# Performance work log

Hardware: AMD Instinct MI355X
Metric: run time of the kernel (lower is better)

## Reference

```python
import jax, jax.numpy as jnp
import numpy as np
from jax import lax

B_SZ = 64
D_MODEL = 768
D_INNER = 1536   # expand * d_model
D_STATE = 16
D_CONV = 4
DT_RANK = 48     # ceil(768/16)
ROWS, COLS = 16, 16
L = ROWS * COLS
LN_EPS = 1e-5


def setup_inputs() -> dict:
    key = jax.random.key(0)
    ks = jax.random.split(key, 16)
    def nrm(k, shape, s):
        return jax.random.normal(k, shape, jnp.float32) * s
    # A_log init as in Mamba: log(arange(1..d_state)) tiled over d_inner
    A_log = jnp.log(jnp.tile(jnp.arange(1, D_STATE + 1, dtype=jnp.float32)[None, :], (D_INNER, 1)))
    # dt bias init: inverse-softplus of dt ~ LogUniform(1e-3, 1e-1)
    def dt_bias_init(k):
        u = jax.random.uniform(k, (D_INNER,), jnp.float32)
        dt = jnp.exp(u * (np.log(0.1) - np.log(0.001)) + np.log(0.001))
        return dt + jnp.log(-jnp.expm1(-dt))
    dt_std = DT_RANK ** -0.5
    return {
        "hidden_states": jax.random.normal(ks[0], (B_SZ, L, D_MODEL), jnp.float32),
        "in_proj_w": nrm(ks[1], (2 * D_INNER, D_MODEL), 0.02),
        "conv_w": nrm(ks[2], (D_INNER, D_CONV), 0.2),
        "conv_bias": nrm(ks[3], (D_INNER,), 0.1),
        "conv_w_b": nrm(ks[4], (D_INNER, D_CONV), 0.2),
        "conv_bias_b": nrm(ks[5], (D_INNER,), 0.1),
        "x_proj_w": nrm(ks[6], (DT_RANK + 2 * D_STATE, D_INNER), 0.02),
        "x_proj_w_b": nrm(ks[7], (DT_RANK + 2 * D_STATE, D_INNER), 0.02),
        "dt_proj_w": jax.random.uniform(ks[8], (D_INNER, DT_RANK), jnp.float32, -dt_std, dt_std),
        "dt_proj_w_b": jax.random.uniform(ks[9], (D_INNER, DT_RANK), jnp.float32, -dt_std, dt_std),
        "dt_bias": dt_bias_init(ks[10]),
        "dt_bias_b": dt_bias_init(ks[11]),
        "A_log": A_log,
        "A_b_log": A_log,
        "Dp": jnp.ones((D_INNER,), jnp.float32),
        "Dp_b": jnp.ones((D_INNER,), jnp.float32),
        "ln_gamma": jnp.ones((D_INNER,), jnp.float32),
        "ln_beta": jnp.zeros((D_INNER,), jnp.float32),
        "out_proj_w": nrm(ks[12], (D_MODEL, D_INNER), 0.02),
    }


def _causal_conv_silu(x, w, b):
    # x: (B, D, L); depthwise causal conv (left-pad K-1) + SiLU
    y = lax.conv_general_dilated(x, w[:, None, :], (1,), [(D_CONV - 1, 0)],
                                 dimension_numbers=("NCH", "OIH", "NCH"),
                                 feature_group_count=D_INNER)
    return jax.nn.silu(y + b[None, :, None])


def _selective_scan(u, dt, A_log, Bm, Cm, dt_bias):
    # u, dt: (B, D, Lr); Bm, Cm: (B, N, Lr)
    A = -jnp.exp(A_log)                                     # (D, N)
    delta = jax.nn.softplus(dt + dt_bias[None, :, None])    # (B, D, Lr)
    dA = jnp.exp(jnp.einsum("bdl,dn->lbdn", delta, A))     # (Lr, B, D, N)
    dBu = jnp.einsum("bdl,bnl,bdl->lbdn", delta, Bm, u)    # (Lr, B, D, N)
    C_l = jnp.moveaxis(Cm, -1, 0)                           # (Lr, B, N)
    def step(h, inp):
        dA_t, dBu_t, C_t = inp
        h = dA_t * h + dBu_t
        return h, jnp.einsum("bdn,bn->bd", h, C_t)
    h0 = jnp.zeros(dA.shape[1:], dA.dtype)
    _, ys = lax.scan(step, h0, (dA, dBu, C_l))
    return jnp.moveaxis(ys, 0, -1)                          # (B, D, Lr)


def _direction(x, conv_w, conv_bias, x_proj_w, dt_proj_w, dt_bias, A_log, Dp):
    xc = _causal_conv_silu(x, conv_w, conv_bias)            # (B, D, L)
    x_comp = xc.reshape(-1, D_INNER, ROWS, COLS).mean(axis=3)  # (B, D, ROWS)
    x_dbl = jnp.einsum("bdl,ed->ble", x_comp, x_proj_w)    # (B, ROWS, R+2N)
    dt, Bm, Cm = jnp.split(x_dbl, [DT_RANK, DT_RANK + D_STATE], axis=-1)
    dt = jnp.einsum("blr,dr->bdl", dt, dt_proj_w)          # (B, D, ROWS)
    Bm = jnp.moveaxis(Bm, 1, 2)                             # (B, N, ROWS)
    Cm = jnp.moveaxis(Cm, 1, 2)
    y = _selective_scan(x_comp, dt, A_log, Bm, Cm, dt_bias)
    return jnp.repeat(y, COLS, axis=2) + Dp[None, :, None] * xc  # (B, D, L)


def reference(hidden_states, in_proj_w, conv_w, conv_bias, conv_w_b, conv_bias_b,
              x_proj_w, x_proj_w_b, dt_proj_w, dt_proj_w_b, dt_bias, dt_bias_b,
              A_log, A_b_log, Dp, Dp_b, ln_gamma, ln_beta, out_proj_w):
    xz = jnp.einsum("bld,ed->bel", hidden_states, in_proj_w)  # (B, 2*Di, L)
    x, z = jnp.split(xz, 2, axis=1)
    out_f = _direction(x, conv_w, conv_bias, x_proj_w, dt_proj_w, dt_bias, A_log, Dp)
    out_b = _direction(x[:, :, ::-1], conv_w_b, conv_bias_b, x_proj_w_b, dt_proj_w_b, dt_bias_b, A_b_log, Dp_b)
    comb = jnp.moveaxis((out_f + out_b[:, :, ::-1]) * 0.5, 1, 2)  # (B, L, Di)
    mu = comb.mean(-1, keepdims=True)
    var = comb.var(-1, keepdims=True)
    normed = (comb - mu) * lax.rsqrt(var + LN_EPS) * ln_gamma + ln_beta
    gated = normed * jax.nn.silu(jnp.moveaxis(z, 1, 2))
    return jnp.einsum("bld,od->blo", gated, out_proj_w)       # (B, L, d_model)
```

## Files before the change

### kernel.cpp

```cpp
#include <hip/hip_runtime.h>
#include <cstdint>
#include <cstddef>

typedef __bf16 bf16_t;
typedef __attribute__((ext_vector_type(2))) __bf16 bf16x2;
typedef __attribute__((ext_vector_type(8))) __bf16 bf16x8;
typedef __attribute__((ext_vector_type(4))) float f32x4;

#define NB     64
#define LSEQ   256
#define DM     768
#define DI     1536
#define NSTATE 16
#define NROWS  16
#define RANK   48

#define BF16_PROBE 0x3F803F80u

__device__ __forceinline__ float bf2f(bf16_t v) { return (float)v; }

__device__ __forceinline__ float ldp(const void* p, size_t i, bool isbf) {
  return isbf ? (float)((const bf16_t*)p)[i] : ((const float*)p)[i];
}

__device__ __forceinline__ float silu_f(float x) {
  const float e = __expf(-fabsf(x));
  return (x >= 0.f) ? (x / (1.f + e)) : (x * e / (1.f + e));
}

__device__ __forceinline__ void async16(const bf16_t* g, bf16_t* l) {
  __builtin_amdgcn_global_load_lds(
      (const __attribute__((address_space(1))) void*)g,
      (__attribute__((address_space(3))) void*)l, 16, 0, 0);
}

__global__ __launch_bounds__(256) void cvt_kernel(
    const void* __restrict__ in, bf16_t* __restrict__ out, int n8,
    const uint32_t* __restrict__ probe)
{
  const int i = blockIdx.x * 256 + threadIdx.x;
  if (i >= n8) return;
  if (probe[0] == BF16_PROBE) {
    ((bf16x8*)out)[i] = ((const bf16x8*)in)[i];
  } else {
    const float* f = (const float*)in + (size_t)i * 8;
    f32x4 lo = *(const f32x4*)f, hi = *(const f32x4*)(f + 4);
    ((bf16x8*)out)[i] = (bf16x8){(bf16_t)lo.x, (bf16_t)lo.y, (bf16_t)lo.z, (bf16_t)lo.w,
                                 (bf16_t)hi.x, (bf16_t)hi.y, (bf16_t)hi.z, (bf16_t)hi.w};
  }
}

#define LDS_IDX(ab, db, half) (((ab) << 2) + ((db) << 1) + (half))

#define STAGE(ab, db, half, kt) do {                                          \
    const int _kt = ((kt) < NT) ? (kt) : (NT - 1);                            \
    const bf16_t* _g = (ab) ? B : A;                                          \
    const size_t _rb = ((ab) ? bn : bm) + (size_t)((half) * 128);             \
    bf16_t* _l = &sm[LDS_IDX(ab, db, half)][0];                               \
    _Pragma("unroll")                                                         \
    for (int _j = 0; _j < 2; _j++) {                                          \
      const int _c = wave * 2 + _j;                                           \
      async16(_g + (_rb + _c * 8 + srow) * (size_t)K + (size_t)_kt * 64 + scol,\
              _l + _c * 512);                                                 \
    }                                                                         \
  } while (0)

#define LOAD_A(db, mg) do {                                                   \
    _Pragma("unroll")                                                         \
    for (int _t = 0; _t < 2; _t++) {                                          \
      const int _mt = (mg) * 2 + _t;                                          \
      const int _lr = _mt * 32 + wm * 16 + r;                                 \
      const bf16_t* _b = &sm[LDS_IDX(0, db, _mt >> 2)][(_lr & 127) * 64];     \
      _Pragma("unroll")                                                       \
      for (int _s = 0; _s < 2; _s++)                                          \
        af[_t][_s] = *(const bf16x8*)&_b[(((_s * 4 + quad) ^ r7) * 8)];       \
    }                                                                         \
  } while (0)

#define LOAD_B(db) do {                                                       \
    _Pragma("unroll")                                                         \
    for (int _nt = 0; _nt < 4; _nt++) {                                       \
      const int _lr = _nt * 64 + wn * 16 + r;                                 \
      const bf16_t* _b = &sm[LDS_IDX(1, db, _lr >> 7)][(_lr & 127) * 64];     \
      _Pragma("unroll")                                                       \
      for (int _s = 0; _s < 2; _s++)                                          \
        bfr[_nt][_s] = *(const bf16x8*)&_b[(((_s * 4 + quad) ^ r7) * 8)];     \
    }                                                                         \
  } while (0)

#define MFMA16(mg) do {                                                       \
    __builtin_amdgcn_s_setprio(1);                                            \
    _Pragma("unroll")                                                         \
    for (int _t = 0; _t < 2; _t++)                                            \
    _Pragma("unroll")                                                         \
    for (int _nt = 0; _nt < 4; _nt++)                                         \
    _Pragma("unroll")                                                         \
    for (int _s = 0; _s < 2; _s++)                                            \
      acc[(mg) * 2 + _t][_nt] = __builtin_amdgcn_mfma_f32_16x16x32_bf16(      \
          af[_t][_s], bfr[_nt][_s], acc[(mg) * 2 + _t][_nt], 0, 0, 0);        \
    __builtin_amdgcn_s_setprio(0);                                            \
  } while (0)

#define BAR()    __builtin_amdgcn_s_barrier()
#define WAITL0() asm volatile("s_waitcnt lgkmcnt(0)" ::: "memory")
#define WAITV6() asm volatile("s_waitcnt vmcnt(6)" ::: "memory")

__global__ __launch_bounds__(512, 2) void gemm256_kernel(
    const bf16_t* __restrict__ A, const bf16_t* __restrict__ B,
    void* __restrict__ C, int M, int N, int K, int cIsF32)
{
  __shared__ bf16_t sm[8][8192];
  const int tid  = threadIdx.x;
  const int wave = tid >> 6, lane = tid & 63;
  const int wm = wave >> 2, wn = wave & 3;
  const int r = lane & 15, quad = lane >> 4, r7 = lane & 7;
  const int srow = lane >> 3;
  const int scol = ((lane & 7) ^ srow) * 8;
  const int NT = K >> 6;

  const int nwg  = gridDim.x * gridDim.y;
  const int orig = blockIdx.y * gridDim.x + blockIdx.x;
  const int swz  = (orig & 7) * (nwg >> 3) + (orig >> 3);
  const size_t bm = (size_t)(swz / gridDim.x) * 256;
  const size_t bn = (size_t)(swz % gridDim.x) * 256;

  f32x4 acc[8][4];
#pragma unroll
  for (int i = 0; i < 8; i++)
#pragma unroll
    for (int j = 0; j < 4; j++) acc[i][j] = (f32x4){0.f, 0.f, 0.f, 0.f};

  bf16x8 af[2][2];
  bf16x8 bfr[4][2];

  STAGE(1, 0, 0, 0);  STAGE(1, 0, 1, 0);  STAGE(0, 0, 0, 0);  STAGE(0, 0, 1, 0);
  asm volatile("s_waitcnt vmcnt(4)" ::: "memory");
  STAGE(1, 1, 0, 1);  STAGE(1, 1, 1, 1);  STAGE(0, 1, 0, 1);
  WAITV6();
  BAR();

  const int NP = NT >> 1;
  for (int i = 0; i < NP; ++i) {
    const int t1 = 2 * i + 1, t2 = 2 * i + 2, t3 = 2 * i + 3;
    LOAD_B(0); LOAD_A(0, 0); STAGE(0, 1, 1, t1);
    BAR(); WAITL0(); MFMA16(0); BAR();

    LOAD_A(0, 1); STAGE(1, 0, 0, t2);
    BAR(); WAITL0(); MFMA16(1); BAR();

    LOAD_A(0, 2); STAGE(1, 0, 1, t2);
    BAR(); WAITL0(); MFMA16(2); BAR();

    LOAD_A(0, 3); STAGE(0, 0, 0, t2);
    WAITV6();
    BAR(); WAITL0(); MFMA16(3); BAR();

    LOAD_B(1); LOAD_A(1, 0); STAGE(0, 0, 1, t2);
    BAR(); WAITL0(); MFMA16(0); BAR();

    LOAD_A(1, 1); STAGE(1, 1, 0, t3);
    BAR(); WAITL0(); MFMA16(1); BAR();

    LOAD_A(1, 2); STAGE(1, 1, 1, t3);
    BAR(); WAITL0(); MFMA16(2); BAR();

    LOAD_A(1, 3); STAGE(0, 1, 0, t3);
    WAITV6();
    BAR(); WAITL0(); MFMA16(3); BAR();
  }

  const int col = lane & 15;
  const int rb4 = quad * 4;
#pragma unroll
  for (int mt = 0; mt < 8; mt++)
#pragma unroll
    for (int nt = 0; nt < 4; nt++)
#pragma unroll
      for (int v = 0; v < 4; v++) {
        const size_t m = bm + mt * 32 + wm * 16 + rb4 + v;
        const size_t n = bn + nt * 64 + wn * 16 + col;
        const size_t ci = m * (size_t)N + n;
        if (cIsF32) ((float*)C)[ci] = acc[mt][nt][v];
        else        ((bf16_t*)C)[ci] = (bf16_t)acc[mt][nt][v];
      }
}

__global__ __launch_bounds__(256) void conv_kernel(
    const bf16_t* __restrict__ xz,
    const void* __restrict__ cw_f, const void* __restrict__ cb_f,
    const void* __restrict__ cw_b, const void* __restrict__ cb_b,
    bf16_t* __restrict__ xc_f, bf16_t* __restrict__ xc_b,
    float* __restrict__ comp_f, float* __restrict__ comp_b,
    const uint32_t* __restrict__ probe)
{
  const bool isbf = (probe[0] == BF16_PROBE);
  const int dir = blockIdx.y;
  int bi = blockIdx.x;
  const int chunk = bi & 3;
  bi >>= 2;
  const int b = bi / 3;
  const int pblk = bi % 3;
  const int d0 = (pblk * 256 + threadIdx.x) * 2;
  const void* cw = dir ? cw_b : cw_f;
  const void* cb = dir ? cb_b : cb_f;
  bf16_t* xc = dir ? xc_b : xc_f;
  float* comp = dir ? comp_b : comp_f;

  const float w00 = ldp(cw, d0 * 4 + 0, isbf), w01 = ldp(cw, d0 * 4 + 1, isbf),
              w02 = ldp(cw, d0 * 4 + 2, isbf), w03 = ldp(cw, d0 * 4 + 3, isbf);
  const float w10 = ldp(cw, (d0 + 1) * 4 + 0, isbf), w11 = ldp(cw, (d0 + 1) * 4 + 1, isbf),
              w12 = ldp(cw, (d0 + 1) * 4 + 2, isbf), w13 = ldp(cw, (d0 + 1) * 4 + 3, isbf);
  const float bias0 = ldp(cb, d0, isbf), bias1 = ldp(cb, d0 + 1, isbf);

  float a3 = 0.f, a2 = 0.f, a1 = 0.f;
  float c3 = 0.f, c2 = 0.f, c1 = 0.f;
  const int lr0 = chunk * 64;
  if (lr0 >= 3) {
#pragma unroll
    for (int i = 3; i >= 1; --i) {
      const int lrp = lr0 - i;
      const int l = dir ? (LSEQ - 1 - lrp) : lrp;
      bf16x2 xv = *(const bf16x2*)(xz + ((size_t)b * LSEQ + l) * (2 * DI) + d0);
      a3 = a2; a2 = a1; a1 = (float)xv.x;
      c3 = c2; c2 = c1; c1 = (float)xv.y;
    }
  }

  float s0 = 0.f, s1 = 0.f;
  for (int lr = lr0; lr < lr0 + 64; ++lr) {
    const int l = dir ? (LSEQ - 1 - lr) : lr;
    bf16x2 xv = *(const bf16x2*)(xz + ((size_t)b * LSEQ + l) * (2 * DI) + d0);
    const float x0 = (float)xv.x, x1 = (float)xv.y;
    float y0 = silu_f(bias0 + w00 * a3 + w01 * a2 + w02 * a1 + w03 * x0);
    float y1 = silu_f(bias1 + w10 * c3 + w11 * c2 + w12 * c1 + w13 * x1);
    a3 = a2; a2 = a1; a1 = x0;
    c3 = c2; c2 = c1; c1 = x1;
    *(bf16x2*)(xc + ((size_t)b * LSEQ + lr) * DI + d0) = (bf16x2){(bf16_t)y0, (bf16_t)y1};
    s0 += y0; s1 += y1;
    if ((lr & 15) == 15) {
      size_t ci = ((size_t)b * NROWS + (lr >> 4)) * DI + d0;
      comp[ci]     = s0 * (1.f / 16.f);
      comp[ci + 1] = s1 * (1.f / 16.f);
      s0 = 0.f; s1 = 0.f;
    }
  }
}

__global__ __launch_bounds__(256) void xproj_kernel(
    const float* __restrict__ comp_f, const float* __restrict__ comp_b,
    const void* __restrict__ w_f, const void* __restrict__ w_b,
    float* __restrict__ xd_f, float* __restrict__ xd_b,
    const uint32_t* __restrict__ probe)
{
  const bool isbf = (probe[0] == BF16_PROBE);
  const int dir = blockIdx.y;
  const int row = blockIdx.x;
  const float* comp = dir ? comp_b : comp_f;
  const void* W = dir ? w_b : w_f;
  float* out = dir ? xd_b : xd_f;

  __shared__ float xrow[DI];
  for (int i = threadIdx.x; i < DI; i += 256) xrow[i] = comp[(size_t)row * DI + i];
  __syncthreads();

  const int wave = threadIdx.x >> 6, lane = threadIdx.x & 63;
  for (int oo = 0; oo < 20; ++oo) {
    const int o = wave * 20 + oo;
    float s = 0.f;
#pragma unroll
    for (int j = 0; j < 24; ++j) {
      const int k = lane + 64 * j;
      s += xrow[k] * ldp(W, (size_t)o * DI + k, isbf);
    }
    for (int off = 32; off; off >>= 1) s += __shfl_down(s, off);
    if (lane == 0) out[(size_t)row * 80 + o] = s;
  }
}

__global__ __launch_bounds__(256) void scan_kernel(
    const float* __restrict__ xd_fg, const float* __restrict__ xd_bg,
    const float* comp_f, const float* comp_b,
    const void* __restrict__ dtw_f, const void* __restrict__ dtw_b,
    const void* __restrict__ dtb_f, const void* __restrict__ dtb_b,
    const void* __restrict__ Al_f, const void* __restrict__ Al_b,
    float* y_fg, float* y_bg,
    const uint32_t* __restrict__ probe)
{
  const bool isbf = (probe[0] == BF16_PROBE);
  const int dir = blockIdx.y;
  const int b = blockIdx.x / 6;
  const int d = (blockIdx.x % 6) * 256 + threadIdx.x;
  const float* xd_g = dir ? xd_bg : xd_fg;
  const float* comp = dir ? comp_b : comp_f;
  const void* dtw = dir ? dtw_b : dtw_f;
  const void* dtb = dir ? dtb_b : dtb_f;
  const void* Al  = dir ? Al_b : Al_f;
  float* y = dir ? y_bg : y_fg;

  __shared__ float xd[NROWS * 80];
  for (int i = threadIdx.x; i < NROWS * 80; i += 256) xd[i] = xd_g[(size_t)b * (NROWS * 80) + i];
  __syncthreads();

  float dt[NROWS];
#pragma unroll
  for (int l = 0; l < NROWS; l++) dt[l] = 0.f;
  for (int r = 0; r < RANK; r++) {
    const float w = ldp(dtw, (size_t)d * RANK + r, isbf);
#pragma unroll
    for (int l = 0; l < NROWS; l++) dt[l] += xd[l * 80 + r] * w;
  }

  float A[NSTATE];
#pragma unroll
  for (int n = 0; n < NSTATE; n++) A[n] = -__expf(ldp(Al, (size_t)d * NSTATE + n, isbf));
  const float bias = ldp(dtb, d, isbf);

  float h[NSTATE];
#pragma unroll
  for (int n = 0; n < NSTATE; n++) h[n] = 0.f;

  for (int l = 0; l < NROWS; l++) {
    const float u = comp[((size_t)b * NROWS + l) * DI + d];
    const float dv = dt[l] + bias;
    const float delta = (dv > 15.f) ? dv : log1pf(__expf(dv));
    const float du = delta * u;
    float yv = 0.f;
#pragma unroll
    for (int n = 0; n < NSTATE; n++) {
      const float hn = __expf(delta * A[n]) * h[n] + du * xd[l * 80 + RANK + n];
      h[n] = hn;
      yv += hn * xd[l * 80 + RANK + NSTATE + n];
    }
    y[((size_t)b * NROWS + l) * DI + d] = yv;
  }
}

__global__ __launch_bounds__(256) void combine_kernel(
    const float* __restrict__ y_f, const float* __restrict__ y_b,
    bf16_t* xcg_f,
    const bf16_t* __restrict__ xc_b,
    const bf16_t* __restrict__ xz,
    const void* __restrict__ Dp, const void* __restrict__ Dp_b,
    const void* __restrict__ gamma, const void* __restrict__ beta,
    const uint32_t* __restrict__ probe)
{
  const bool isbf = (probe[0] == BF16_PROBE);
  const int m = blockIdx.x;
  const int b = m >> 8, l = m & 255;
  const int lr = LSEQ - 1 - l;
  const int tid = threadIdx.x;

  float v[6];
  float sum = 0.f, sq = 0.f;
#pragma unroll
  for (int i = 0; i < 6; i++) {
    const int d = tid + i * 256;
    const float cf = bf2f(xcg_f[((size_t)b * LSEQ + l) * DI + d]);
    const float cb = bf2f(xc_b[((size_t)b * LSEQ + lr) * DI + d]);
    const float vf = y_f[((size_t)b * NROWS + (l >> 4)) * DI + d] + ldp(Dp, d, isbf) * cf;
    const float vb = y_b[((size_t)b * NROWS + (lr >> 4)) * DI + d] + ldp(Dp_b, d, isbf) * cb;
    const float c = 0.5f * (vf + vb);
    v[i] = c; sum += c; sq += c * c;
  }
  for (int off = 32; off; off >>= 1) {
    sum += __shfl_down(sum, off);
    sq  += __shfl_down(sq, off);
  }
  __shared__ float rs[4], rq[4];
  if ((tid & 63) == 0) { rs[tid >> 6] = sum; rq[tid >> 6] = sq; }
  __syncthreads();
  const float S  = rs[0] + rs[1] + rs[2] + rs[3];
  const float SQ = rq[0] + rq[1] + rq[2] + rq[3];
  const float mu = S * (1.f / (float)DI);
  const float var = fmaxf(SQ * (1.f / (float)DI) - mu * mu, 0.f);
  const float rstd = rsqrtf(var + 1e-5f);
#pragma unroll
  for (int i = 0; i < 6; i++) {
    const int d = tid + i * 256;
    const float nrm = (v[i] - mu) * rstd * ldp(gamma, d, isbf) + ldp(beta, d, isbf);
    const float z = bf2f(xz[((size_t)b * LSEQ + l) * (2 * DI) + DI + d]);
    xcg_f[(size_t)m * DI + d] = (bf16_t)(nrm * silu_f(z));
  }
}

extern "C" void kernel_launch(void* const* d_in, const int* in_sizes, int n_in,
                              void* d_out, int out_size, void* d_ws, size_t ws_size,
                              hipStream_t stream)
{
  (void)in_sizes; (void)n_in; (void)out_size; (void)ws_size;
  const void* H     = d_in[0];
  const void* Win   = d_in[1];
  const void* cw_f  = d_in[2];
  const void* cb_f  = d_in[3];
  const void* cw_b  = d_in[4];
  const void* cb_b  = d_in[5];
  const void* xpw_f = d_in[6];
  const void* xpw_b = d_in[7];
  const void* dtw_f = d_in[8];
  const void* dtw_b = d_in[9];
  const void* dtb_f = d_in[10];
  const void* dtb_b = d_in[11];
  const void* Al_f  = d_in[12];
  const void* Al_b  = d_in[13];
  const void* Dp    = d_in[14];
  const void* Dp_b  = d_in[15];
  const void* gam   = d_in[16];
  const void* bet   = d_in[17];
  const void* Wout  = d_in[18];
  const uint32_t* probe = (const uint32_t*)d_in[14];

  const size_t M = (size_t)NB * LSEQ;
  char* ws = (char*)d_ws;
  bf16_t* xz    = (bf16_t*)ws;  ws += M * (2 * DI) * sizeof(bf16_t);
  bf16_t* xc_f  = (bf16_t*)ws;  ws += M * DI * sizeof(bf16_t);
  bf16_t* xc_b  = (bf16_t*)ws;  ws += M * DI * sizeof(bf16_t);
  float* comp_f = (float*)ws;   ws += (size_t)NB * NROWS * DI * sizeof(float);
  float* comp_b = (float*)ws;   ws += (size_t)NB * NROWS * DI * sizeof(float);
  float* xd_f   = (float*)ws;   ws += (size_t)NB * NROWS * 80 * sizeof(float);
  float* xd_b   = (float*)ws;   ws += (size_t)NB * NROWS * 80 * sizeof(float);
  bf16_t* Hb    = (bf16_t*)ws;  ws += M * DM * sizeof(bf16_t);
  bf16_t* Winb  = (bf16_t*)ws;  ws += (size_t)(2 * DI) * DM * sizeof(bf16_t);
  bf16_t* Woutb = (bf16_t*)ws;  ws += (size_t)DM * DI * sizeof(bf16_t);

  cvt_kernel<<<(int)((M * DM / 8 + 255) / 256), 256, 0, stream>>>(H, Hb, (int)(M * DM / 8), probe);
  cvt_kernel<<<(2 * DI * DM / 8 + 255) / 256, 256, 0, stream>>>(Win, Winb, 2 * DI * DM / 8, probe);
  cvt_kernel<<<(DM * DI / 8 + 255) / 256, 256, 0, stream>>>(Wout, Woutb, DM * DI / 8, probe);

  gemm256_kernel<<<dim3(2 * DI / 256, M / 256), 512, 0, stream>>>(
      Hb, Winb, xz, (int)M, 2 * DI, DM, 0);

  conv_kernel<<<dim3(768, 2), 256, 0, stream>>>(
      xz, cw_f, cb_f, cw_b, cb_b, xc_f, xc_b, comp_f, comp_b, probe);

  xproj_kernel<<<dim3(NB * NROWS, 2), 256, 0, stream>>>(
      comp_f, comp_b, xpw_f, xpw_b, xd_f, xd_b, probe);

  scan_kernel<<<dim3(NB * (DI / 256), 2), 256, 0, stream>>>(
      xd_f, xd_b, comp_f, comp_b, dtw_f, dtw_b, dtb_f, dtb_b, Al_f, Al_b,
      comp_f, comp_b, probe);

  combine_kernel<<<dim3(NB * LSEQ), 256, 0, stream>>>(
      comp_f, comp_b, xc_f, xc_b, xz, Dp, Dp_b, gam, bet, probe);

  gemm256_kernel<<<dim3(DM / 256, M / 256), 512, 0, stream>>>(
      xc_f, Woutb, d_out, (int)M, DM, DI, 1);
}
```

Before: 478.1 us.

## Fuse causal conv and row pooling into in-projection GEMM epilogue

The in-projection GEMM epilogue now transposes the x-half tile through LDS and runs the forward and backward depthwise causal conv, SiLU and 16-step pooling directly, writing xc and comp. The z-half is stored as a compact bf16 buffer, so the full xz intermediate and the separate conv kernel are gone. The dt_proj weights are also pre-transposed to fp32 so the scan reads them coalesced. In exchange the GEMM epilogue gets heavier and serial per thread, and the enlarged LDS footprint (about 132KB) may reduce occupancy relative to the two-blocks-per-CU launch bound.

```diff
diff --git a/kernel.cpp b/kernel.cpp
--- a/kernel.cpp
+++ b/kernel.cpp
@@ -6,6 +6,7 @@
 typedef __attribute__((ext_vector_type(2))) __bf16 bf16x2;
 typedef __attribute__((ext_vector_type(8))) __bf16 bf16x8;
 typedef __attribute__((ext_vector_type(4))) float f32x4;
+typedef __attribute__((ext_vector_type(2))) float f32x2;
 
 #define NB     64
 #define LSEQ   256
@@ -48,6 +49,17 @@
     ((bf16x8*)out)[i] = (bf16x8){(bf16_t)lo.x, (bf16_t)lo.y, (bf16_t)lo.z, (bf16_t)lo.w,
                                  (bf16_t)hi.x, (bf16_t)hi.y, (bf16_t)hi.z, (bf16_t)hi.w};
   }
+}
+
+__global__ __launch_bounds__(256) void dtwt_kernel(
+    const void* __restrict__ dtw, float* __restrict__ out,
+    const uint32_t* __restrict__ probe)
+{
+  const bool isbf = (probe[0] == BF16_PROBE);
+  const int i = blockIdx.x * 256 + threadIdx.x;
+  if (i >= RANK * DI) return;
+  const int r = i / DI, d = i - r * DI;
+  out[i] = ldp(dtw, (size_t)d * RANK + r, isbf);
 }
 
 #define LDS_IDX(ab, db, half) (((ab) << 2) + ((db) << 1) + (half))
@@ -107,9 +119,17 @@
 
 __global__ __launch_bounds__(512, 2) void gemm256_kernel(
     const bf16_t* __restrict__ A, const bf16_t* __restrict__ B,
-    void* __restrict__ C, int M, int N, int K, int cIsF32)
-{
-  __shared__ bf16_t sm[8][8192];
+    void* __restrict__ C, int M, int N, int K, int mode,
+    bf16_t* __restrict__ xc_f, bf16_t* __restrict__ xc_b,
+    float* __restrict__ comp_f, float* __restrict__ comp_b,
+    const void* __restrict__ cw_f, const void* __restrict__ cb_f,
+    const void* __restrict__ cw_b, const void* __restrict__ cb_b,
+    const uint32_t* __restrict__ probe)
+{
+  __shared__ __align__(16) char smraw[256 * 258 * 2];
+  typedef bf16_t row8k_t[8192];
+  row8k_t* sm = (row8k_t*)smraw;
+
   const int tid  = threadIdx.x;
   const int wave = tid >> 6, lane = tid & 63;
   const int wm = wave >> 2, wn = wave & 3;
@@ -169,79 +189,109 @@
     BAR(); WAITL0(); MFMA16(3); BAR();
   }
 
-  const int col = lane & 15;
+  const int col16 = lane & 15;
   const int rb4 = quad * 4;
-#pragma unroll
-  for (int mt = 0; mt < 8; mt++)
-#pragma unroll
-    for (int nt = 0; nt < 4; nt++)
-#pragma unroll
-      for (int v = 0; v < 4; v++) {
-        const size_t m = bm + mt * 32 + wm * 16 + rb4 + v;
-        const size_t n = bn + nt * 64 + wn * 16 + col;
-        const size_t ci = m * (size_t)N + n;
-        if (cIsF32) ((float*)C)[ci] = acc[mt][nt][v];
-        else        ((bf16_t*)C)[ci] = (bf16_t)acc[mt][nt][v];
+
+  if (mode == 0) {
+#pragma unroll
+    for (int mt = 0; mt < 8; mt++)
+#pragma unroll
+      for (int nt = 0; nt < 4; nt++)
+#pragma unroll
+        for (int v = 0; v < 4; v++) {
+          const size_t m = bm + mt * 32 + wm * 16 + rb4 + v;
+          const size_t n = bn + nt * 64 + wn * 16 + col16;
+          ((float*)C)[m * (size_t)N + n] = acc[mt][nt][v];
+        }
+  } else if (bn >= (size_t)DI) {
+    bf16_t* zb = (bf16_t*)C;
+    const size_t zc = bn - DI;
+#pragma unroll
+    for (int mt = 0; mt < 8; mt++)
+#pragma unroll
+      for (int nt = 0; nt < 4; nt++)
+#pragma unroll
+        for (int v = 0; v < 4; v++) {
+          const size_t m = bm + mt * 32 + wm * 16 + rb4 + v;
+          zb[m * DI + zc + nt * 64 + wn * 16 + col16] = (bf16_t)acc[mt][nt][v];
+        }
+  } else {
+    asm volatile("s_waitcnt vmcnt(0)" ::: "memory");
+    __syncthreads();
+    bf16_t* xt = (bf16_t*)smraw;
+#pragma unroll
+    for (int mt = 0; mt < 8; mt++) {
+      const int mrow = mt * 32 + wm * 16 + rb4;
+#pragma unroll
+      for (int nt = 0; nt < 4; nt++) {
+        const int ccol = nt * 64 + wn * 16 + col16;
+        bf16_t* qp = &xt[ccol * 258 + mrow];
+        *(bf16x2*)qp       = (bf16x2){(bf16_t)acc[mt][nt][0], (bf16_t)acc[mt][nt][1]};
+        *(bf16x2*)(qp + 2) = (bf16x2){(bf16_t)acc[mt][nt][2], (bf16_t)acc[mt][nt][3]};
       }
-}
-
-__global__ __launch_bounds__(256) void conv_kernel(
-    const bf16_t* __restrict__ xz,
-    const void* __restrict__ cw_f, const void* __restrict__ cb_f,
-    const void* __restrict__ cw_b, const void* __restrict__ cb_b,
-    bf16_t* __restrict__ xc_f, bf16_t* __restrict__ xc_b,
-    float* __restrict__ comp_f, float* __restrict__ comp_b,
-    const uint32_t* __restrict__ probe)
-{
-  const bool isbf = (probe[0] == BF16_PROBE);
-  const int dir = blockIdx.y;
-  int bi = blockIdx.x;
-  const int chunk = bi & 3;
-  bi >>= 2;
-  const int b = bi / 3;
-  const int pblk = bi % 3;
-  const int d0 = (pblk * 256 + threadIdx.x) * 2;
-  const void* cw = dir ? cw_b : cw_f;
-  const void* cb = dir ? cb_b : cb_f;
-  bf16_t* xc = dir ? xc_b : xc_f;
-  float* comp = dir ? comp_b : comp_f;
-
-  const float w00 = ldp(cw, d0 * 4 + 0, isbf), w01 = ldp(cw, d0 * 4 + 1, isbf),
-              w02 = ldp(cw, d0 * 4 + 2, isbf), w03 = ldp(cw, d0 * 4 + 3, isbf);
-  const float w10 = ldp(cw, (d0 + 1) * 4 + 0, isbf), w11 = ldp(cw, (d0 + 1) * 4 + 1, isbf),
-              w12 = ldp(cw, (d0 + 1) * 4 + 2, isbf), w13 = ldp(cw, (d0 + 1) * 4 + 3, isbf);
-  const float bias0 = ldp(cb, d0, isbf), bias1 = ldp(cb, d0 + 1, isbf);
-
-  float a3 = 0.f, a2 = 0.f, a1 = 0.f;
-  float c3 = 0.f, c2 = 0.f, c1 = 0.f;
-  const int lr0 = chunk * 64;
-  if (lr0 >= 3) {
-#pragma unroll
-    for (int i = 3; i >= 1; --i) {
-      const int lrp = lr0 - i;
-      const int l = dir ? (LSEQ - 1 - lrp) : lrp;
-      bf16x2 xv = *(const bf16x2*)(xz + ((size_t)b * LSEQ + l) * (2 * DI) + d0);
-      a3 = a2; a2 = a1; a1 = (float)xv.x;
-      c3 = c2; c2 = c1; c1 = (float)xv.y;
     }
-  }
-
-  float s0 = 0.f, s1 = 0.f;
-  for (int lr = lr0; lr < lr0 + 64; ++lr) {
-    const int l = dir ? (LSEQ - 1 - lr) : lr;
-    bf16x2 xv = *(const bf16x2*)(xz + ((size_t)b * LSEQ + l) * (2 * DI) + d0);
-    const float x0 = (float)xv.x, x1 = (float)xv.y;
-    float y0 = silu_f(bias0 + w00 * a3 + w01 * a2 + w02 * a1 + w03 * x0);
-    float y1 = silu_f(bias1 + w10 * c3 + w11 * c2 + w12 * c1 + w13 * x1);
-    a3 = a2; a2 = a1; a1 = x0;
-    c3 = c2; c2 = c1; c1 = x1;
-    *(bf16x2*)(xc + ((size_t)b * LSEQ + lr) * DI + d0) = (bf16x2){(bf16_t)y0, (bf16_t)y1};
-    s0 += y0; s1 += y1;
-    if ((lr & 15) == 15) {
-      size_t ci = ((size_t)b * NROWS + (lr >> 4)) * DI + d0;
-      comp[ci]     = s0 * (1.f / 16.f);
-      comp[ci + 1] = s1 * (1.f / 16.f);
-      s0 = 0.f; s1 = 0.f;
+    __syncthreads();
+
+    const bool isbf = (probe[0] == BF16_PROBE);
+    const int p  = tid & 127;
+    const int qq = tid >> 7;
+    const int c0 = p * 2;
+    const int r0 = qq * 64;
+    const int dg = (int)bn + c0;
+    const int bidx = (int)(bm >> 8);
+    const bf16_t* x0 = &xt[c0 * 258];
+    const bf16_t* x1 = &xt[(c0 + 1) * 258];
+
+#pragma unroll
+    for (int dir = 0; dir < 2; ++dir) {
+      const void* cw = dir ? cw_b : cw_f;
+      const void* cb = dir ? cb_b : cb_f;
+      bf16_t* xc  = dir ? xc_b : xc_f;
+      float* comp = dir ? comp_b : comp_f;
+      const float wa0 = ldp(cw, (size_t)dg * 4 + 0, isbf),
+                  wa1 = ldp(cw, (size_t)dg * 4 + 1, isbf),
+                  wa2 = ldp(cw, (size_t)dg * 4 + 2, isbf),
+                  wa3 = ldp(cw, (size_t)dg * 4 + 3, isbf);
+      const float wb0 = ldp(cw, (size_t)(dg + 1) * 4 + 0, isbf),
+                  wb1 = ldp(cw, (size_t)(dg + 1) * 4 + 1, isbf),
+                  wb2 = ldp(cw, (size_t)(dg + 1) * 4 + 2, isbf),
+                  wb3 = ldp(cw, (size_t)(dg + 1) * 4 + 3, isbf);
+      const float ba = ldp(cb, dg, isbf), bb = ldp(cb, dg + 1, isbf);
+      float a1 = 0.f, a2 = 0.f, a3 = 0.f, b1 = 0.f, b2 = 0.f, b3 = 0.f;
+      if (r0 > 0) {
+        if (dir == 0) {
+          a1 = (float)x0[r0 - 1]; a2 = (float)x0[r0 - 2]; a3 = (float)x0[r0 - 3];
+          b1 = (float)x1[r0 - 1]; b2 = (float)x1[r0 - 2]; b3 = (float)x1[r0 - 3];
+        } else {
+          a1 = (float)x0[256 - r0]; a2 = (float)x0[257 - r0]; a3 = (float)x0[258 - r0];
+          b1 = (float)x1[256 - r0]; b2 = (float)x1[257 - r0]; b3 = (float)x1[258 - r0];
+        }
+      }
+      float sa = 0.f, sb = 0.f;
+      for (int rr = 0; rr < 64; rr += 2) {
+        const int lr = r0 + rr;
+        const int row = dir ? (254 - lr) : lr;
+        const bf16x2 va = *(const bf16x2*)&x0[row];
+        const bf16x2 vb = *(const bf16x2*)&x1[row];
+        const float xaf = dir ? (float)va.y : (float)va.x;
+        const float xas = dir ? (float)va.x : (float)va.y;
+        const float xbf = dir ? (float)vb.y : (float)vb.x;
+        const float xbs = dir ? (float)vb.x : (float)vb.y;
+        const float ya0 = silu_f(ba + wa0 * a3 + wa1 * a2 + wa2 * a1 + wa3 * xaf);
+        const float yb0 = silu_f(bb + wb0 * b3 + wb1 * b2 + wb2 * b1 + wb3 * xbf);
+        a3 = a2; a2 = a1; a1 = xaf;  b3 = b2; b2 = b1; b1 = xbf;
+        const float ya1 = silu_f(ba + wa0 * a3 + wa1 * a2 + wa2 * a1 + wa3 * xas);
+        const float yb1 = silu_f(bb + wb0 * b3 + wb1 * b2 + wb2 * b1 + wb3 * xbs);
+        a3 = a2; a2 = a1; a1 = xas;  b3 = b2; b2 = b1; b1 = xbs;
+        *(bf16x2*)&xc[((size_t)(bm + lr)) * DI + dg]     = (bf16x2){(bf16_t)ya0, (bf16_t)yb0};
+        *(bf16x2*)&xc[((size_t)(bm + lr + 1)) * DI + dg] = (bf16x2){(bf16_t)ya1, (bf16_t)yb1};
+        sa += ya0 + ya1; sb += yb0 + yb1;
+        if ((rr & 15) == 14) {
+          *(f32x2*)&comp[((size_t)bidx * NROWS + (lr >> 4)) * DI + dg] =
+              (f32x2){sa * (1.f / 16.f), sb * (1.f / 16.f)};
+          sa = 0.f; sb = 0.f;
+        }
+      }
     }
   }
 }
@@ -280,7 +330,7 @@
 __global__ __launch_bounds__(256) void scan_kernel(
     const float* __restrict__ xd_fg, const float* __restrict__ xd_bg,
     const float* comp_f, const float* comp_b,
-    const void* __restrict__ dtw_f, const void* __restrict__ dtw_b,
+    const float* __restrict__ dtwT_f, const float* __restrict__ dtwT_b,
     const void* __restrict__ dtb_f, const void* __restrict__ dtb_b,
     const void* __restrict__ Al_f, const void* __restrict__ Al_b,
     float* y_fg, float* y_bg,
@@ -292,7 +342,7 @@
   const int d = (blockIdx.x % 6) * 256 + threadIdx.x;
   const float* xd_g = dir ? xd_bg : xd_fg;
   const float* comp = dir ? comp_b : comp_f;
-  const void* dtw = dir ? dtw_b : dtw_f;
+  const float* dtwT = dir ? dtwT_b : dtwT_f;
   const void* dtb = dir ? dtb_b : dtb_f;
   const void* Al  = dir ? Al_b : Al_f;
   float* y = dir ? y_bg : y_fg;
@@ -305,7 +355,7 @@
 #pragma unroll
   for (int l = 0; l < NROWS; l++) dt[l] = 0.f;
   for (int r = 0; r < RANK; r++) {
-    const float w = ldp(dtw, (size_t)d * RANK + r, isbf);
+    const float w = dtwT[(size_t)r * DI + d];
 #pragma unroll
     for (int l = 0; l < NROWS; l++) dt[l] += xd[l * 80 + r] * w;
   }
@@ -339,7 +389,7 @@
     const float* __restrict__ y_f, const float* __restrict__ y_b,
     bf16_t* xcg_f,
     const bf16_t* __restrict__ xc_b,
-    const bf16_t* __restrict__ xz,
+    const bf16_t* __restrict__ zb,
     const void* __restrict__ Dp, const void* __restrict__ Dp_b,
     const void* __restrict__ gamma, const void* __restrict__ beta,
     const uint32_t* __restrict__ probe)
@@ -378,7 +428,7 @@
   for (int i = 0; i < 6; i++) {
     const int d = tid + i * 256;
     const float nrm = (v[i] - mu) * rstd * ldp(gamma, d, isbf) + ldp(beta, d, isbf);
-    const float z = bf2f(xz[((size_t)b * LSEQ + l) * (2 * DI) + DI + d]);
+    const float z = bf2f(zb[(size_t)m * DI + d]);
     xcg_f[(size_t)m * DI + d] = (bf16_t)(nrm * silu_f(z));
   }
 }
@@ -411,7 +461,7 @@
 
   const size_t M = (size_t)NB * LSEQ;
   char* ws = (char*)d_ws;
-  bf16_t* xz    = (bf16_t*)ws;  ws += M * (2 * DI) * sizeof(bf16_t);
+  bf16_t* zb    = (bf16_t*)ws;  ws += M * DI * sizeof(bf16_t);
   bf16_t* xc_f  = (bf16_t*)ws;  ws += M * DI * sizeof(bf16_t);
   bf16_t* xc_b  = (bf16_t*)ws;  ws += M * DI * sizeof(bf16_t);
   float* comp_f = (float*)ws;   ws += (size_t)NB * NROWS * DI * sizeof(float);
@@ -421,27 +471,30 @@
   bf16_t* Hb    = (bf16_t*)ws;  ws += M * DM * sizeof(bf16_t);
   bf16_t* Winb  = (bf16_t*)ws;  ws += (size_t)(2 * DI) * DM * sizeof(bf16_t);
   bf16_t* Woutb = (bf16_t*)ws;  ws += (size_t)DM * DI * sizeof(bf16_t);
+  float* dtwT_f = (float*)ws;   ws += (size_t)RANK * DI * sizeof(float);
+  float* dtwT_b = (float*)ws;   ws += (size_t)RANK * DI * sizeof(float);
 
   cvt_kernel<<<(int)((M * DM / 8 + 255) / 256), 256, 0, stream>>>(H, Hb, (int)(M * DM / 8), probe);
   cvt_kernel<<<(2 * DI * DM / 8 + 255) / 256, 256, 0, stream>>>(Win, Winb, 2 * DI * DM / 8, probe);
   cvt_kernel<<<(DM * DI / 8 + 255) / 256, 256, 0, stream>>>(Wout, Woutb, DM * DI / 8, probe);
+  dtwt_kernel<<<(RANK * DI + 255) / 256, 256, 0, stream>>>(dtw_f, dtwT_f, probe);
+  dtwt_kernel<<<(RANK * DI + 255) / 256, 256, 0, stream>>>(dtw_b, dtwT_b, probe);
 
   gemm256_kernel<<<dim3(2 * DI / 256, M / 256), 512, 0, stream>>>(
-      Hb, Winb, xz, (int)M, 2 * DI, DM, 0);
-
-  conv_kernel<<<dim3(768, 2), 256, 0, stream>>>(
-      xz, cw_f, cb_f, cw_b, cb_b, xc_f, xc_b, comp_f, comp_b, probe);
+      Hb, Winb, zb, (int)M, 2 * DI, DM, 1,
+      xc_f, xc_b, comp_f, comp_b, cw_f, cb_f, cw_b, cb_b, probe);
 
   xproj_kernel<<<dim3(NB * NROWS, 2), 256, 0, stream>>>(
       comp_f, comp_b, xpw_f, xpw_b, xd_f, xd_b, probe);
 
   scan_kernel<<<dim3(NB * (DI / 256), 2), 256, 0, stream>>>(
-      xd_f, xd_b, comp_f, comp_b, dtw_f, dtw_b, dtb_f, dtb_b, Al_f, Al_b,
+      xd_f, xd_b, comp_f, comp_b, dtwT_f, dtwT_b, dtb_f, dtb_b, Al_f, Al_b,
       comp_f, comp_b, probe);
 
   combine_kernel<<<dim3(NB * LSEQ), 256, 0, stream>>>(
-      comp_f, comp_b, xc_f, xc_b, xz, Dp, Dp_b, gam, bet, probe);
+      comp_f, comp_b, xc_f, xc_b, zb, Dp, Dp_b, gam, bet, probe);
 
   gemm256_kernel<<<dim3(DM / 256, M / 256), 512, 0, stream>>>(
-      xc_f, Woutb, d_out, (int)M, DM, DI, 1);
-}
+      xc_f, Woutb, d_out, (int)M, DM, DI, 0,
+      nullptr, nullptr, nullptr, nullptr, nullptr, nullptr, nullptr, nullptr, probe);
+}
```

New measurement: 470.0 us. About the same (-1.7%).

## Split in-proj output into x/z buffers and fuse both conv directions into one pass

Applied to the files above, without the earlier changes.

The in-projection GEMM epilogue now writes the x half and z half into separate contiguous [M, DI] bf16 buffers. The conv kernel loads each x value once and computes both the forward and the reversed-direction causal conv from the same sliding window, halving its grid and its reads of x. The combine kernel reads z from the dense buffer. This cuts redundant global reads and improves stride, at the cost of a more complex conv loop with three extra halo iterations per chunk.

```diff
diff --git a/kernel.cpp b/kernel.cpp
--- a/kernel.cpp
+++ b/kernel.cpp
@@ -6,6 +6,7 @@
 typedef __attribute__((ext_vector_type(2))) __bf16 bf16x2;
 typedef __attribute__((ext_vector_type(8))) __bf16 bf16x8;
 typedef __attribute__((ext_vector_type(4))) float f32x4;
+typedef __attribute__((ext_vector_type(2))) float f32x2;
 
 #define NB     64
 #define LSEQ   256
@@ -107,7 +108,8 @@
 
 __global__ __launch_bounds__(512, 2) void gemm256_kernel(
     const bf16_t* __restrict__ A, const bf16_t* __restrict__ B,
-    void* __restrict__ C, int M, int N, int K, int cIsF32)
+    void* __restrict__ C, int M, int N, int K, int mode,
+    bf16_t* __restrict__ xb)
 {
   __shared__ bf16_t sm[8][8192];
   const int tid  = threadIdx.x;
@@ -169,24 +171,37 @@
     BAR(); WAITL0(); MFMA16(3); BAR();
   }
 
-  const int col = lane & 15;
+  const int col16 = lane & 15;
   const int rb4 = quad * 4;
-#pragma unroll
-  for (int mt = 0; mt < 8; mt++)
-#pragma unroll
-    for (int nt = 0; nt < 4; nt++)
-#pragma unroll
-      for (int v = 0; v < 4; v++) {
-        const size_t m = bm + mt * 32 + wm * 16 + rb4 + v;
-        const size_t n = bn + nt * 64 + wn * 16 + col;
-        const size_t ci = m * (size_t)N + n;
-        if (cIsF32) ((float*)C)[ci] = acc[mt][nt][v];
-        else        ((bf16_t*)C)[ci] = (bf16_t)acc[mt][nt][v];
-      }
+
+  if (mode == 0) {
+#pragma unroll
+    for (int mt = 0; mt < 8; mt++)
+#pragma unroll
+      for (int nt = 0; nt < 4; nt++)
+#pragma unroll
+        for (int v = 0; v < 4; v++) {
+          const size_t m = bm + mt * 32 + wm * 16 + rb4 + v;
+          const size_t n = bn + nt * 64 + wn * 16 + col16;
+          ((float*)C)[m * (size_t)N + n] = acc[mt][nt][v];
+        }
+  } else {
+    bf16_t* dst = (bn < (size_t)DI) ? xb : (bf16_t*)C;
+    const size_t cb0 = (bn < (size_t)DI) ? bn : bn - DI;
+#pragma unroll
+    for (int mt = 0; mt < 8; mt++)
+#pragma unroll
+      for (int nt = 0; nt < 4; nt++)
+#pragma unroll
+        for (int v = 0; v < 4; v++) {
+          const size_t m = bm + mt * 32 + wm * 16 + rb4 + v;
+          dst[m * DI + cb0 + nt * 64 + wn * 16 + col16] = (bf16_t)acc[mt][nt][v];
+        }
+  }
 }
 
 __global__ __launch_bounds__(256) void conv_kernel(
-    const bf16_t* __restrict__ xz,
+    const bf16_t* __restrict__ xb,
     const void* __restrict__ cw_f, const void* __restrict__ cb_f,
     const void* __restrict__ cw_b, const void* __restrict__ cb_b,
     bf16_t* __restrict__ xc_f, bf16_t* __restrict__ xc_b,
@@ -194,54 +209,77 @@
     const uint32_t* __restrict__ probe)
 {
   const bool isbf = (probe[0] == BF16_PROBE);
-  const int dir = blockIdx.y;
   int bi = blockIdx.x;
   const int chunk = bi & 3;
   bi >>= 2;
   const int b = bi / 3;
   const int pblk = bi % 3;
   const int d0 = (pblk * 256 + threadIdx.x) * 2;
-  const void* cw = dir ? cw_b : cw_f;
-  const void* cb = dir ? cb_b : cb_f;
-  bf16_t* xc = dir ? xc_b : xc_f;
-  float* comp = dir ? comp_b : comp_f;
-
-  const float w00 = ldp(cw, d0 * 4 + 0, isbf), w01 = ldp(cw, d0 * 4 + 1, isbf),
-              w02 = ldp(cw, d0 * 4 + 2, isbf), w03 = ldp(cw, d0 * 4 + 3, isbf);
-  const float w10 = ldp(cw, (d0 + 1) * 4 + 0, isbf), w11 = ldp(cw, (d0 + 1) * 4 + 1, isbf),
-              w12 = ldp(cw, (d0 + 1) * 4 + 2, isbf), w13 = ldp(cw, (d0 + 1) * 4 + 3, isbf);
-  const float bias0 = ldp(cb, d0, isbf), bias1 = ldp(cb, d0 + 1, isbf);
-
-  float a3 = 0.f, a2 = 0.f, a1 = 0.f;
-  float c3 = 0.f, c2 = 0.f, c1 = 0.f;
   const int lr0 = chunk * 64;
-  if (lr0 >= 3) {
-#pragma unroll
-    for (int i = 3; i >= 1; --i) {
-      const int lrp = lr0 - i;
-      const int l = dir ? (LSEQ - 1 - lrp) : lrp;
-      bf16x2 xv = *(const bf16x2*)(xz + ((size_t)b * LSEQ + l) * (2 * DI) + d0);
-      a3 = a2; a2 = a1; a1 = (float)xv.x;
-      c3 = c2; c2 = c1; c1 = (float)xv.y;
+
+  const float wf0a = ldp(cw_f, (size_t)d0 * 4 + 0, isbf),
+              wf1a = ldp(cw_f, (size_t)d0 * 4 + 1, isbf),
+              wf2a = ldp(cw_f, (size_t)d0 * 4 + 2, isbf),
+              wf3a = ldp(cw_f, (size_t)d0 * 4 + 3, isbf);
+  const float wf0c = ldp(cw_f, (size_t)(d0 + 1) * 4 + 0, isbf),
+              wf1c = ldp(cw_f, (size_t)(d0 + 1) * 4 + 1, isbf),
+              wf2c = ldp(cw_f, (size_t)(d0 + 1) * 4 + 2, isbf),
+              wf3c = ldp(cw_f, (size_t)(d0 + 1) * 4 + 3, isbf);
+  const float wb0a = ldp(cw_b, (size_t)d0 * 4 + 0, isbf),
+              wb1a = ldp(cw_b, (size_t)d0 * 4 + 1, isbf),
+              wb2a = ldp(cw_b, (size_t)d0 * 4 + 2, isbf),
+              wb3a = ldp(cw_b, (size_t)d0 * 4 + 3, isbf);
+  const float wb0c = ldp(cw_b, (size_t)(d0 + 1) * 4 + 0, isbf),
+              wb1c = ldp(cw_b, (size_t)(d0 + 1) * 4 + 1, isbf),
+              wb2c = ldp(cw_b, (size_t)(d0 + 1) * 4 + 2, isbf),
+              wb3c = ldp(cw_b, (size_t)(d0 + 1) * 4 + 3, isbf);
+  const float bfa = ldp(cb_f, d0, isbf), bfc = ldp(cb_f, d0 + 1, isbf);
+  const float bba = ldp(cb_b, d0, isbf), bbc = ldp(cb_b, d0 + 1, isbf);
+
+  const bf16_t* xrow = xb + (size_t)b * LSEQ * DI + d0;
+
+  float t0a = 0.f, t1a = 0.f, t2a = 0.f, t3a = 0.f;
+  float t0c = 0.f, t1c = 0.f, t2c = 0.f, t3c = 0.f;
+  if (lr0 > 0) {
+    bf16x2 v;
+    v = *(const bf16x2*)&xrow[(size_t)(lr0 - 3) * DI]; t1a = (float)v.x; t1c = (float)v.y;
+    v = *(const bf16x2*)&xrow[(size_t)(lr0 - 2) * DI]; t2a = (float)v.x; t2c = (float)v.y;
+    v = *(const bf16x2*)&xrow[(size_t)(lr0 - 1) * DI]; t3a = (float)v.x; t3c = (float)v.y;
+  }
+
+  float sfa = 0.f, sfc = 0.f;
+  float sba = 0.f, sbc = 0.f;
+  for (int l = lr0; l < lr0 + 67; ++l) {
+    float xa = 0.f, xcv = 0.f;
+    if (l < LSEQ) {
+      bf16x2 v = *(const bf16x2*)&xrow[(size_t)l * DI];
+      xa = (float)v.x; xcv = (float)v.y;
     }
-  }
-
-  float s0 = 0.f, s1 = 0.f;
-  for (int lr = lr0; lr < lr0 + 64; ++lr) {
-    const int l = dir ? (LSEQ - 1 - lr) : lr;
-    bf16x2 xv = *(const bf16x2*)(xz + ((size_t)b * LSEQ + l) * (2 * DI) + d0);
-    const float x0 = (float)xv.x, x1 = (float)xv.y;
-    float y0 = silu_f(bias0 + w00 * a3 + w01 * a2 + w02 * a1 + w03 * x0);
-    float y1 = silu_f(bias1 + w10 * c3 + w11 * c2 + w12 * c1 + w13 * x1);
-    a3 = a2; a2 = a1; a1 = x0;
-    c3 = c2; c2 = c1; c1 = x1;
-    *(bf16x2*)(xc + ((size_t)b * LSEQ + lr) * DI + d0) = (bf16x2){(bf16_t)y0, (bf16_t)y1};
-    s0 += y0; s1 += y1;
-    if ((lr & 15) == 15) {
-      size_t ci = ((size_t)b * NROWS + (lr >> 4)) * DI + d0;
-      comp[ci]     = s0 * (1.f / 16.f);
-      comp[ci + 1] = s1 * (1.f / 16.f);
-      s0 = 0.f; s1 = 0.f;
+    t0a = t1a; t1a = t2a; t2a = t3a; t3a = xa;
+    t0c = t1c; t1c = t2c; t2c = t3c; t3c = xcv;
+
+    if (l < lr0 + 64) {
+      const float ya = silu_f(bfa + wf0a * t0a + wf1a * t1a + wf2a * t2a + wf3a * t3a);
+      const float yc = silu_f(bfc + wf0c * t0c + wf1c * t1c + wf2c * t2c + wf3c * t3c);
+      *(bf16x2*)&xc_f[((size_t)b * LSEQ + l) * DI + d0] = (bf16x2){(bf16_t)ya, (bf16_t)yc};
+      sfa += ya; sfc += yc;
+      if ((l & 15) == 15) {
+        *(f32x2*)&comp_f[((size_t)b * NROWS + (l >> 4)) * DI + d0] =
+            (f32x2){sfa * (1.f / 16.f), sfc * (1.f / 16.f)};
+        sfa = 0.f; sfc = 0.f;
+      }
+    }
+    if (l >= lr0 + 3) {
+      const int j = 258 - l;
+      const float ya = silu_f(bba + wb0a * t3a + wb1a * t2a + wb2a * t1a + wb3a * t0a);
+      const float yc = silu_f(bbc + wb0c * t3c + wb1c * t2c + wb2c * t1c + wb3c * t0c);
+      *(bf16x2*)&xc_b[((size_t)b * LSEQ + j) * DI + d0] = (bf16x2){(bf16_t)ya, (bf16_t)yc};
+      sba += ya; sbc += yc;
+      if ((j & 15) == 0) {
+        *(f32x2*)&comp_b[((size_t)b * NROWS + (j >> 4)) * DI + d0] =
+            (f32x2){sba * (1.f / 16.f), sbc * (1.f / 16.f)};
+        sba = 0.f; sbc = 0.f;
+      }
     }
   }
 }
@@ -339,7 +377,7 @@
     const float* __restrict__ y_f, const float* __restrict__ y_b,
     bf16_t* xcg_f,
     const bf16_t* __restrict__ xc_b,
-    const bf16_t* __restrict__ xz,
+    const bf16_t* __restrict__ zb,
     const void* __restrict__ Dp, const void* __restrict__ Dp_b,
     const void* __restrict__ gamma, const void* __restrict__ beta,
     const uint32_t* __restrict__ probe)
@@ -378,7 +416,7 @@
   for (int i = 0; i < 6; i++) {
     const int d = tid + i * 256;
     const float nrm = (v[i] - mu) * rstd * ldp(gamma, d, isbf) + ldp(beta, d, isbf);
-    const float z = bf2f(xz[((size_t)b * LSEQ + l) * (2 * DI) + DI + d]);
+    const float z = bf2f(zb[(size_t)m * DI + d]);
     xcg_f[(size_t)m * DI + d] = (bf16_t)(nrm * silu_f(z));
   }
 }
@@ -411,7 +449,8 @@
 
   const size_t M = (size_t)NB * LSEQ;
   char* ws = (char*)d_ws;
-  bf16_t* xz    = (bf16_t*)ws;  ws += M * (2 * DI) * sizeof(bf16_t);
+  bf16_t* zb    = (bf16_t*)ws;  ws += M * DI * sizeof(bf16_t);
+  bf16_t* xb    = (bf16_t*)ws;  ws += M * DI * sizeof(bf16_t);
   bf16_t* xc_f  = (bf16_t*)ws;  ws += M * DI * sizeof(bf16_t);
   bf16_t* xc_b  = (bf16_t*)ws;  ws += M * DI * sizeof(bf16_t);
   float* comp_f = (float*)ws;   ws += (size_t)NB * NROWS * DI * sizeof(float);
@@ -427,10 +466,10 @@
   cvt_kernel<<<(DM * DI / 8 + 255) / 256, 256, 0, stream>>>(Wout, Woutb, DM * DI / 8, probe);
 
   gemm256_kernel<<<dim3(2 * DI / 256, M / 256), 512, 0, stream>>>(
-      Hb, Winb, xz, (int)M, 2 * DI, DM, 0);
-
-  conv_kernel<<<dim3(768, 2), 256, 0, stream>>>(
-      xz, cw_f, cb_f, cw_b, cb_b, xc_f, xc_b, comp_f, comp_b, probe);
+      Hb, Winb, zb, (int)M, 2 * DI, DM, 1, xb);
+
+  conv_kernel<<<dim3(768), 256, 0, stream>>>(
+      xb, cw_f, cb_f, cw_b, cb_b, xc_f, xc_b, comp_f, comp_b, probe);
 
   xproj_kernel<<<dim3(NB * NROWS, 2), 256, 0, stream>>>(
       comp_f, comp_b, xpw_f, xpw_b, xd_f, xd_b, probe);
@@ -440,8 +479,8 @@
       comp_f, comp_b, probe);
 
   combine_kernel<<<dim3(NB * LSEQ), 256, 0, stream>>>(
-      comp_f, comp_b, xc_f, xc_b, xz, Dp, Dp_b, gam, bet, probe);
+      comp_f, comp_b, xc_f, xc_b, zb, Dp, Dp_b, gam, bet, probe);
 
   gemm256_kernel<<<dim3(DM / 256, M / 256), 512, 0, stream>>>(
-      xc_f, Woutb, d_out, (int)M, DM, DI, 1);
-}
+      xc_f, Woutb, d_out, (int)M, DM, DI, 0, nullptr);
+}
```

Measured after the change: 482.7 us. Within noise of the previous version (+1.0%).
